# Kernel tuning notes

Measured on AMD Instinct MI355X. Metric: run time of the kernel, lower is better.

The kernel has to match this reference:

```python
import jax, jax.numpy as jnp
import numpy as np

B, CIN, COUT, L, K = 4, 512, 512, 4096, 7
DIL, STR = 1, 1
OUT_LEN = (L - DIL * (K - 1) - 1) // STR + 1  # 4090 ('valid' conv output length)


def setup_inputs() -> dict:
    key = jax.random.key(0)
    k1, k2, k3, k4 = jax.random.split(key, 4)
    x = jax.random.normal(k1, (B, CIN, L), dtype=jnp.float32)
    offsets = jax.random.normal(k2, (B, 1, OUT_LEN, K), dtype=jnp.float32)
    # kaiming_uniform_(a=sqrt(5)) on [COUT, CIN, K] -> U(-1/sqrt(fan_in), 1/sqrt(fan_in))
    fan_in = CIN * K
    bound = 1.0 / np.sqrt(fan_in)
    weight = jax.random.uniform(k3, (COUT, CIN, K), dtype=jnp.float32, minval=-bound, maxval=bound)
    bias = jax.random.uniform(k4, (COUT,), dtype=jnp.float32, minval=-bound, maxval=bound)
    return {"x": x, "offsets": offsets, "weight": weight, "bias": bias}


def _deform_interp(x, offsets, kernel_size, dilation, stride):
    # x: [B, C, L]; offsets: [B, 1, out_len, K] (offset_groups == 1)
    Lx = x.shape[-1]
    dil_pos = (jnp.arange(kernel_size) * dilation).astype(offsets.dtype)       # [K]
    out_len = offsets.shape[-2]
    t0s = (jnp.arange(out_len) * stride).astype(offsets.dtype)[:, None]        # [out_len, 1]
    T = t0s + dil_pos + offsets                                                # [B, 1, out_len, K]
    # constrained: each sample must stay inside its receptive field
    T = jnp.maximum(T, t0s)
    T = jnp.minimum(T, t0s + dil_pos[-1])
    U0 = jnp.clip(jnp.floor(T).astype(jnp.int32), 0, Lx - 2)                   # [B, 1, out_len, K]
    U = jnp.stack([U0, U0 + 1], axis=-1)                                       # [B, 1, out_len, K, 2]
    idx = U[:, 0]                                                              # [B, out_len, K, 2]
    # gather along length, broadcast index over channels
    xg = jax.vmap(lambda xb, ib: xb[:, ib])(x, idx)                            # [B, C, out_len, K, 2]
    # linear-interp weights: max(0, 1 - |U - T|)
    G = jnp.maximum(0.0, 1.0 - jnp.abs(U.astype(T.dtype) - T[..., None]))      # [B, 1, out_len, K, 2]
    return jnp.sum(G * xg, axis=-1)                                            # [B, C, out_len, K]


def reference(x, offsets, weight, bias):
    samp = _deform_interp(x, offsets, K, DIL, STR)                             # [B, C, out_len, K]
    # conv1d(weight, stride=K) on flattened [B, C, out_len*K] == per-position full contraction
    out = jnp.einsum('bcok,dck->bdo', samp, weight) + bias[:, None]            # [B, COUT, out_len]
    return out
```

## Files before the change

### kernel.cpp

```cpp
#include <hip/hip_runtime.h>
#include <hip/hip_bf16.h>
#include <stdint.h>

#define B_      4
#define CIN     512
#define COUT    512
#define L_      4096
#define K_      7
#define OUT_LEN 4090

typedef unsigned short ushort_t;
typedef __attribute__((ext_vector_type(8))) __bf16 bf16x8;
typedef __attribute__((ext_vector_type(4))) float f32x4;

__device__ __forceinline__ uint32_t f2bf(float f) {
    uint32_t u = __float_as_uint(f);
    return (u + 0x7fffu + ((u >> 16) & 1u)) >> 16;
}

__device__ __forceinline__ uint32_t pack2bf(float s0, float s1) {
    __hip_bfloat162 h = __float22bfloat162_rn(make_float2(s0, s1));
    uint32_t r;
    __builtin_memcpy(&r, &h, 4);
    return r;
}

__device__ __forceinline__ uint32_t interp1(uint32_t wl, uint32_t wh, float g0, float g1) {
    const float l0 = __uint_as_float(wl << 16);
    const float l1 = __uint_as_float(wl & 0xffff0000u);
    const float h0 = __uint_as_float(wh << 16);
    const float h1 = __uint_as_float(wh & 0xffff0000u);
    return pack2bf(g0 * l0 + g1 * h0, g0 * l1 + g1 * h1);
}

__device__ __forceinline__ void async16(const void* g, void* l) {
    __builtin_amdgcn_global_load_lds(
        (const __attribute__((address_space(1))) unsigned int*)g,
        (__attribute__((address_space(3))) unsigned int*)l, 16, 0, 0);
}


__global__ __launch_bounds__(256)
void reorder_w2_kernel(const float* __restrict__ w, uint32_t* __restrict__ Wr) {
    const int d   = blockIdx.x;
    const int tid = threadIdx.x;
    __shared__ float wrow[3584];
    const float4* src = (const float4*)(w + (size_t)d * 3584);
    for (int e = tid; e < 896; e += 256) ((float4*)wrow)[e] = src[e];
    __syncthreads();
    const int cc  = tid >> 4;
    const int clp = tid & 15;
    const int pos = (((clp >> 2) ^ ((d >> 1) & 3)) << 2) | (clp & 3);
    #pragma unroll
    for (int k = 0; k < K_; ++k) {
        const float w0 = wrow[tid * 14 + k];
        const float w1 = wrow[tid * 14 + 7 + k];
        Wr[((size_t)(cc * 7 + k) * 512 + d) * 16 + pos] = (f2bf(w1) << 16) | f2bf(w0);
    }
}

__global__ __launch_bounds__(256)
void interp_pack_kernel(const float* __restrict__ x, const float* __restrict__ offs,
                        uint32_t* __restrict__ P) {
    const int obx = blockIdx.x;
    const int cc  = blockIdx.y;
    const int b   = blockIdx.z;
    const int tid = threadIdx.x;
    const int o0  = obx * 128;
    __shared__ __align__(16) uint32_t XT[2176];

    const float* xc = x + ((size_t)b * CIN + cc * 32) * L_ + o0;
    #pragma unroll
    for (int r = 0; r < 3; ++r) {
        const int e = r * 256 + tid;
        if (e < 544) {
            const int cp   = e / 34;
            const int col4 = e - cp * 34;
            const int colb = col4 * 4;
            const float* p0 = xc + (size_t)(2 * cp) * L_ + colb;
            const float* p1 = p0 + L_;
            float4 v0, v1;
            if (o0 + colb + 3 < L_) {
                v0 = *(const float4*)p0;
                v1 = *(const float4*)p1;
            } else {
                float a0 = (o0 + colb + 0 < L_) ? p0[0] : 0.f;
                float a1 = (o0 + colb + 1 < L_) ? p0[1] : 0.f;
                float a2 = (o0 + colb + 2 < L_) ? p0[2] : 0.f;
                float a3 = (o0 + colb + 3 < L_) ? p0[3] : 0.f;
                float b0 = (o0 + colb + 0 < L_) ? p1[0] : 0.f;
                float b1 = (o0 + colb + 1 < L_) ? p1[1] : 0.f;
                float b2 = (o0 + colb + 2 < L_) ? p1[2] : 0.f;
                float b3 = (o0 + colb + 3 < L_) ? p1[3] : 0.f;
                v0 = make_float4(a0, a1, a2, a3);
                v1 = make_float4(b0, b1, b2, b3);
            }
            const float* f0 = (const float*)&v0;
            const float* f1 = (const float*)&v1;
            const int cpg = cp >> 1, hh = cp & 1;
            #pragma unroll
            for (int ii = 0; ii < 4; ++ii) {
                const int col = colb + ii;
                XT[col * 16 + (((cpg ^ (col & 7)) << 1) | hh)] = pack2bf(f0[ii], f1[ii]);
            }
        }
    }
    __syncthreads();

    const int o_loc = tid >> 1;
    const int h     = tid & 1;
    int o = o0 + o_loc; if (o > OUT_LEN - 1) o = OUT_LEN - 1;
    const float t0f = (float)o;
    const int sr = (o_loc >> 1) & 3;
    uint32_t* Pb = P + ((size_t)((b * 16 + cc) * 7) * 32 + obx) * 2048 + o_loc * 16;
    const int c0 = ((2 * h) ^ sr) << 2;
    const int c1 = ((2 * h + 1) ^ sr) << 2;
    #pragma unroll
    for (int k = 0; k < K_; ++k) {
        const float off = offs[((size_t)b * OUT_LEN + o) * K_ + k];
        float T = t0f + (float)k + off;
        T = fmaxf(T, t0f);
        T = fminf(T, t0f + 6.0f);
        int u0 = (int)floorf(T); if (u0 > L_ - 2) u0 = L_ - 2;
        const float g1 = T - (float)u0;
        const float g0 = 1.0f - g1;
        const int ul = u0 - o0;
        const uint32_t* R0 = &XT[ul * 16];
        const uint32_t* R1 = &XT[(ul + 1) * 16];
        const int s0 = ul & 7, s1 = (ul + 1) & 7;
        uint32_t ow[8];
        #pragma unroll
        for (int q = 0; q < 4; ++q) {
            const int pg = h * 4 + q;
            const uint2 lo = *(const uint2*)&R0[(pg ^ s0) << 1];
            const uint2 hi = *(const uint2*)&R1[(pg ^ s1) << 1];
            ow[q * 2 + 0] = interp1(lo.x, hi.x, g0, g1);
            ow[q * 2 + 1] = interp1(lo.y, hi.y, g0, g1);
        }
        uint32_t* Pk = Pb + (size_t)k * 65536;
        *(uint4*)&Pk[c0] = make_uint4(ow[0], ow[1], ow[2], ow[3]);
        *(uint4*)&Pk[c1] = make_uint4(ow[4], ow[5], ow[6], ow[7]);
    }
}

__global__ __launch_bounds__(256, 2)
void gemm_kernel(const ushort_t* __restrict__ Wr, const uint32_t* __restrict__ P,
                 const float* __restrict__ bias, float* __restrict__ out) {
    const int bxi  = blockIdx.x;
    const int o0   = bxi * 128;
    const int d0   = blockIdx.y * 128;
    const int b    = blockIdx.z;
    const int tid  = threadIdx.x;
    const int wv   = tid >> 6;
    const int lane = tid & 63;
    const int m16  = lane & 15;
    const int quad = lane >> 4;
    const int wd   = wv >> 1;
    const int wo   = wv & 1;
    const int sw   = (m16 >> 1) & 3;
    const int chk  = (quad ^ sw) * 8;

    __shared__ __align__(16) ushort_t As0[4096], As1[4096], As2[4096], As3[4096];
    __shared__ __align__(16) ushort_t Bs0[4096], Bs1[4096], Bs2[4096], Bs3[4096];

    const int aoff = (wd * 64 + m16) * 32 + chk;
    const int boff = (wo * 64 + m16) * 32 + chk;

    const ushort_t* Ag = Wr + (size_t)d0 * 32 + (size_t)tid * 8;
    const uint32_t* Bg = P + ((size_t)(b * 112) * 32 + bxi) * 2048 + (size_t)tid * 4;

#define NISSUE_A(S, ASP)                                                          \
    { _Pragma("unroll") for (int r_ = 0; r_ < 2; ++r_)                            \
        async16(Ag + (size_t)(S) * 16384 + r_ * 2048,                             \
                (void*)((ASP) + (r_ * 256 + wv * 64) * 8)); }

#define NISSUE_B(S, BSP)                                                          \
    { _Pragma("unroll") for (int r_ = 0; r_ < 2; ++r_)                            \
        async16(Bg + (size_t)(S) * 65536 + r_ * 1024,                             \
                (void*)((BSP) + (r_ * 256 + wv * 64) * 8)); }

#define NSTEP(ASP, BSP)                                                           \
    {                                                                             \
        bf16x8 af_[4], bf_[4];                                                    \
        _Pragma("unroll")                                                         \
        for (int i_ = 0; i_ < 4; ++i_) af_[i_] = *(const bf16x8*)&(ASP)[aoff + i_ * 512]; \
        _Pragma("unroll")                                                         \
        for (int j_ = 0; j_ < 4; ++j_) bf_[j_] = *(const bf16x8*)&(BSP)[boff + j_ * 512]; \
        _Pragma("unroll")                                                         \
        for (int i_ = 0; i_ < 4; ++i_) {                                          \
            _Pragma("unroll")                                                     \
            for (int j_ = 0; j_ < 4; ++j_)                                        \
                acc[i_][j_] = __builtin_amdgcn_mfma_f32_16x16x32_bf16(af_[i_], bf_[j_], acc[i_][j_], 0, 0, 0); \
        }                                                                         \
    }

    f32x4 acc[4][4];
    #pragma unroll
    for (int i = 0; i < 4; ++i) {
        #pragma unroll
        for (int j = 0; j < 4; ++j) acc[i][j] = (f32x4){0.f, 0.f, 0.f, 0.f};
    }

    NISSUE_A(0, As0); NISSUE_B(0, Bs0);
    NISSUE_A(1, As1); NISSUE_B(1, Bs1);
    __syncthreads();

    #pragma unroll 1
    for (int s = 0; s < 112; s += 8) {
        NISSUE_A(s + 2, As2); NISSUE_B(s + 2, Bs2); NISSUE_A(s + 3, As3); NISSUE_B(s + 3, Bs3);
        NSTEP(As0, Bs0); NSTEP(As1, Bs1); __syncthreads();
        NISSUE_A(s + 4, As0); NISSUE_B(s + 4, Bs0); NISSUE_A(s + 5, As1); NISSUE_B(s + 5, Bs1);
        NSTEP(As2, Bs2); NSTEP(As3, Bs3); __syncthreads();
        NISSUE_A(s + 6, As2); NISSUE_B(s + 6, Bs2); NISSUE_A(s + 7, As3); NISSUE_B(s + 7, Bs3);
        NSTEP(As0, Bs0); NSTEP(As1, Bs1); __syncthreads();
        if (s + 8 < 112) {
            NISSUE_A(s + 8, As0); NISSUE_B(s + 8, Bs0); NISSUE_A(s + 9, As1); NISSUE_B(s + 9, Bs1);
        }
        NSTEP(As2, Bs2); NSTEP(As3, Bs3); __syncthreads();
    }

    #pragma unroll
    for (int i = 0; i < 4; ++i) {
        const int dd = d0 + wd * 64 + i * 16 + quad * 4;
        float bv[4];
        #pragma unroll
        for (int r = 0; r < 4; ++r) bv[r] = bias[dd + r];
        #pragma unroll
        for (int j = 0; j < 4; ++j) {
            const int oo = o0 + wo * 64 + j * 16 + m16;
            if (oo < OUT_LEN) {
                float* op = out + (size_t)b * COUT * OUT_LEN + (size_t)dd * OUT_LEN + oo;
                #pragma unroll
                for (int r = 0; r < 4; ++r)
                    op[(size_t)r * OUT_LEN] = acc[i][j][r] + bv[r];
            }
        }
    }
#undef NISSUE_A
#undef NISSUE_B
#undef NSTEP
}


__global__ __launch_bounds__(256)
void reorder_w1_kernel(const float* __restrict__ w, uint32_t* __restrict__ Wr) {
    const int d   = blockIdx.x;
    const int tid = threadIdx.x;
    __shared__ float wrow[3584];
    const float4* src = (const float4*)(w + (size_t)d * 3584);
    for (int e = tid; e < 896; e += 256) ((float4*)wrow)[e] = src[e];
    __syncthreads();
    const int cc  = tid >> 4;
    const int clp = tid & 15;
    #pragma unroll
    for (int k = 0; k < K_; ++k) {
        const float w0 = wrow[tid * 14 + k];
        const float w1 = wrow[tid * 14 + 7 + k];
        Wr[((size_t)((k * 16 + cc) * 512 + d)) * 16 + clp] = (f2bf(w1) << 16) | f2bf(w0);
    }
}

__global__ __launch_bounds__(256)
void prepack_kernel(const float* __restrict__ x, uint32_t* __restrict__ xpack) {
    const int obx = blockIdx.x;
    const int cc  = blockIdx.y;
    const int b   = blockIdx.z;
    const int tid = threadIdx.x;
    const int o0  = obx * 128;
    __shared__ __align__(16) uint32_t XT[2176];
    const float* xc = x + ((size_t)b * CIN + cc * 32) * L_ + o0;
    #pragma unroll
    for (int r = 0; r < 3; ++r) {
        const int e = r * 256 + tid;
        if (e < 544) {
            const int cp   = e / 34;
            const int col4 = e - cp * 34;
            const int colb = col4 * 4;
            const float* p0 = xc + (size_t)(2 * cp) * L_ + colb;
            const float* p1 = p0 + L_;
            float4 v0, v1;
            if (o0 + colb + 3 < L_) {
                v0 = *(const float4*)p0;
                v1 = *(const float4*)p1;
            } else {
                float a0 = (o0 + colb + 0 < L_) ? p0[0] : 0.f;
                float a1 = (o0 + colb + 1 < L_) ? p0[1] : 0.f;
                float a2 = (o0 + colb + 2 < L_) ? p0[2] : 0.f;
                float a3 = (o0 + colb + 3 < L_) ? p0[3] : 0.f;
                float b0 = (o0 + colb + 0 < L_) ? p1[0] : 0.f;
                float b1 = (o0 + colb + 1 < L_) ? p1[1] : 0.f;
                float b2 = (o0 + colb + 2 < L_) ? p1[2] : 0.f;
                float b3 = (o0 + colb + 3 < L_) ? p1[3] : 0.f;
                v0 = make_float4(a0, a1, a2, a3);
                v1 = make_float4(b0, b1, b2, b3);
            }
            const float* f0 = (const float*)&v0;
            const float* f1 = (const float*)&v1;
            const int cpg = cp >> 1, h = cp & 1;
            #pragma unroll
            for (int ii = 0; ii < 4; ++ii) {
                const int col = colb + ii;
                XT[col * 16 + (((cpg ^ (col & 7)) << 1) | h)] = pack2bf(f0[ii], f1[ii]);
            }
        }
    }
    __syncthreads();
    uint4* dst = (uint4*)xpack + (size_t)((b * 16 + cc) * 32 + obx) * 544;
    const uint4* s4 = (const uint4*)XT;
    #pragma unroll
    for (int r = 0; r < 3; ++r) {
        const int e = r * 256 + tid;
        if (e < 544) dst[e] = s4[e];
    }
}

__global__ __launch_bounds__(256, 2)
void fused_v1_kernel(const float* __restrict__ offs, const ushort_t* __restrict__ Wr,
                     const uint32_t* __restrict__ xpack, const float* __restrict__ bias,
                     float* __restrict__ out) {
    const int bxi  = blockIdx.x;
    const int o0   = bxi * 128;
    const int d0   = blockIdx.y * 128;
    const int b    = blockIdx.z;
    const int tid  = threadIdx.x;
    const int wv   = tid >> 6;
    const int lane = tid & 63;
    const int m16  = lane & 15;
    const int quad = lane >> 4;
    const int ob   = wv * 32;
    const int q2   = quad * 2;

    __shared__ __align__(16) ushort_t As0[4096], As1[4096], As2[4096], As3[4096];
    __shared__ __align__(16) uint32_t XTB0[2304], XTB1[2304];
    __shared__ int    SU[896];
    __shared__ float2 PG[896];

#define ISSUE_A(KK, CC, ASP)                                                      \
    {                                                                             \
        _Pragma("unroll")                                                         \
        for (int r_ = 0; r_ < 2; ++r_) {                                          \
            const int c_ = r_ * 256 + tid;                                        \
            const int row_ = c_ >> 2, pc_ = c_ & 3;                               \
            const ushort_t* g_ = Wr                                               \
                + ((size_t)(((KK) * 16 + (CC)) * 512 + d0 + row_)) * 32 + pc_ * 8;\
            async16(g_, (void*)((ASP) + (r_ * 256 + wv * 64) * 8));               \
        }                                                                         \
    }

#define ISSUE_XTB(CC, XP)                                                         \
    {                                                                             \
        const uint32_t* sp_ = xpack + ((size_t)((b * 16 + (CC)) * 32 + bxi)) * 2176; \
        _Pragma("unroll")                                                         \
        for (int r_ = 0; r_ < 3; ++r_) {                                          \
            const int cb_ = r_ * 256 + wv * 64;                                   \
            if (cb_ < 544) {                                                      \
                const int c_ = r_ * 256 + tid;                                    \
                async16((const void*)(sp_ + (size_t)c_ * 4),                      \
                        (void*)((XP) + (size_t)cb_ * 4));                         \
            }                                                                     \
        }                                                                         \
    }

#define STEP(KK, XP, ASP)                                                         \
    {                                                                             \
        bf16x8 af_[8];                                                            \
        _Pragma("unroll")                                                         \
        for (int i_ = 0; i_ < 8; ++i_)                                            \
            af_[i_] = *(const bf16x8*)&(ASP)[(i_ * 16 + m16) * 32 + quad * 8];    \
        bf16x8 bfr_[2];                                                           \
        _Pragma("unroll")                                                         \
        for (int j_ = 0; j_ < 2; ++j_) {                                          \
            const int row_ = ((KK) << 7) | (ob + j_ * 16 + m16);                  \
            const int u_ = SU[row_];                                              \
            const float2 g_ = PG[row_];                                           \
            const uint32_t* Xr0_ = &(XP)[u_ * 16];                                \
            const uint32_t* Xr1_ = Xr0_ + 16;                                     \
            const int s0_ = u_ & 7, s1_ = (u_ + 1) & 7;                           \
            const uint2 a0_ = *(const uint2*)&Xr0_[((q2     ^ s0_) << 1)];        \
            const uint2 a1_ = *(const uint2*)&Xr0_[(((q2+1) ^ s0_) << 1)];        \
            const uint2 c0_ = *(const uint2*)&Xr1_[((q2     ^ s1_) << 1)];        \
            const uint2 c1_ = *(const uint2*)&Xr1_[(((q2+1) ^ s1_) << 1)];        \
            uint4 rr_;                                                            \
            rr_.x = interp1(a0_.x, c0_.x, g_.x, g_.y);                            \
            rr_.y = interp1(a0_.y, c0_.y, g_.x, g_.y);                            \
            rr_.z = interp1(a1_.x, c1_.x, g_.x, g_.y);                            \
            rr_.w = interp1(a1_.y, c1_.y, g_.x, g_.y);                            \
            __builtin_memcpy(&bfr_[j_], &rr_, 16);                                \
        }                                                                         \
        _Pragma("unroll")                                                         \
        for (int i_ = 0; i_ < 8; ++i_) {                                          \
            _Pragma("unroll")                                                     \
            for (int j_ = 0; j_ < 2; ++j_)                                        \
                acc[i_][j_] = __builtin_amdgcn_mfma_f32_16x16x32_bf16(af_[i_], bfr_[j_], acc[i_][j_], 0, 0, 0); \
        }                                                                         \
    }

#define HALF(CCB, A0_, A1_, A2_, A3_)                                             \
    ISSUE_A(2, (CCB), A2_); ISSUE_A(3, (CCB), A3_); ISSUE_XTB((CCB) + 1, XTB1);   \
    STEP(0, XTB0, A0_); STEP(1, XTB0, A1_); __syncthreads();                      \
    ISSUE_A(4, (CCB), A0_); ISSUE_A(5, (CCB), A1_);                               \
    STEP(2, XTB0, A2_); STEP(3, XTB0, A3_); __syncthreads();                      \
    ISSUE_A(6, (CCB), A2_); ISSUE_A(0, (CCB) + 1, A3_);                           \
    STEP(4, XTB0, A0_); STEP(5, XTB0, A1_); __syncthreads();                      \
    ISSUE_A(1, (CCB) + 1, A0_); ISSUE_A(2, (CCB) + 1, A1_);                       \
    STEP(6, XTB0, A2_); STEP(0, XTB1, A3_); __syncthreads();                      \
    ISSUE_A(3, (CCB) + 1, A2_); ISSUE_A(4, (CCB) + 1, A3_);                       \
    if ((CCB) + 2 < 16) { ISSUE_XTB((CCB) + 2, XTB0); }                           \
    STEP(1, XTB1, A0_); STEP(2, XTB1, A1_); __syncthreads();                      \
    ISSUE_A(5, (CCB) + 1, A0_); ISSUE_A(6, (CCB) + 1, A1_);                       \
    STEP(3, XTB1, A2_); STEP(4, XTB1, A3_); __syncthreads();                      \
    if ((CCB) + 2 < 16) { ISSUE_A(0, (CCB) + 2, A2_); ISSUE_A(1, (CCB) + 2, A3_); } \
    STEP(5, XTB1, A0_); STEP(6, XTB1, A1_); __syncthreads();

    f32x4 acc[8][2];
    #pragma unroll
    for (int i = 0; i < 8; ++i) {
        #pragma unroll
        for (int j = 0; j < 2; ++j) acc[i][j] = (f32x4){0.f, 0.f, 0.f, 0.f};
    }

    ISSUE_XTB(0, XTB0);
    ISSUE_A(0, 0, As0);
    ISSUE_A(1, 0, As1);
    for (int e = tid; e < 896; e += 256) {
        const int k  = e >> 7;
        const int ol = e & 127;
        int o = o0 + ol; if (o > OUT_LEN - 1) o = OUT_LEN - 1;
        const float t0  = (float)o;
        const float off = offs[((size_t)b * OUT_LEN + o) * K_ + k];
        float T = t0 + (float)k + off;
        T = fmaxf(T, t0);
        T = fminf(T, t0 + 6.0f);
        int u0 = (int)floorf(T);
        if (u0 > L_ - 2) u0 = L_ - 2;
        const float g0 = fmaxf(1.0f - fabsf((float)u0 - T), 0.0f);
        const float g1 = fmaxf(1.0f - fabsf((float)(u0 + 1) - T), 0.0f);
        SU[e] = u0 - o0;
        PG[e] = make_float2(g0, g1);
    }
    __syncthreads();

    #pragma unroll 1
    for (int s4 = 0; s4 < 16; s4 += 4) {
        HALF(s4,     As0, As1, As2, As3)
        HALF(s4 + 2, As2, As3, As0, As1)
    }

    #pragma unroll
    for (int i = 0; i < 8; ++i) {
        const int dd = d0 + i * 16 + quad * 4;
        float bv[4];
        #pragma unroll
        for (int r = 0; r < 4; ++r) bv[r] = bias[dd + r];
        #pragma unroll
        for (int j = 0; j < 2; ++j) {
            const int oo = o0 + ob + j * 16 + m16;
            if (oo < OUT_LEN) {
                float* op = out + (size_t)b * COUT * OUT_LEN + (size_t)dd * OUT_LEN + oo;
                #pragma unroll
                for (int r = 0; r < 4; ++r)
                    op[(size_t)r * OUT_LEN] = acc[i][j][r] + bv[r];
            }
        }
    }
#undef ISSUE_A
#undef ISSUE_XTB
#undef STEP
#undef HALF
}

#define BM 64
#define BN 64
#define BC 8
#define TT (BC * K_)

__global__ __launch_bounds__(256, 2)
void deform_conv1d_fallback(const float* __restrict__ x, const float* __restrict__ offsets,
                            const float* __restrict__ weight, const float* __restrict__ bias,
                            float* __restrict__ out) {
    const int o0 = blockIdx.x * BN, d0 = blockIdx.y * BM, b = blockIdx.z, tid = threadIdx.x;
    __shared__ int   SU[BN * K_];
    __shared__ float SG0[BN * K_], SG1[BN * K_];
    __shared__ float XT[BC][BN + 8];
    __shared__ float S[BC][K_][BN];
    __shared__ float WT[BM][TT + 1];
    for (int e = tid; e < BN * K_; e += 256) {
        const int ol = e / K_, k = e % K_, o = o0 + ol;
        int u0rel = 0; float g0 = 0.f, g1 = 0.f;
        if (o < OUT_LEN) {
            const float t0 = (float)o;
            const float off = offsets[(size_t)b * OUT_LEN * K_ + (size_t)o * K_ + k];
            float T = fminf(fmaxf(t0 + (float)k + off, t0), t0 + 6.0f);
            int u0 = (int)floorf(T); if (u0 > L_ - 2) u0 = L_ - 2;
            g0 = fmaxf(1.0f - fabsf((float)u0 - T), 0.0f);
            g1 = fmaxf(1.0f - fabsf((float)(u0 + 1) - T), 0.0f);
            u0rel = u0 - o0;
        }
        SU[e] = u0rel; SG0[e] = g0; SG1[e] = g1;
    }
    float acc[4][4];
    #pragma unroll
    for (int i = 0; i < 4; ++i) {
        #pragma unroll
        for (int j = 0; j < 4; ++j) acc[i][j] = 0.f;
    }
    const int ty = tid >> 4, tx = tid & 15;
    const float* xb = x + (size_t)b * CIN * L_;
    for (int c0 = 0; c0 < CIN; c0 += BC) {
        __syncthreads();
        for (int e = tid; e < BC * (BN + 7); e += 256) {
            const int cl = e / (BN + 7), j = e % (BN + 7), pos = o0 + j;
            XT[cl][j] = (pos < L_) ? xb[(size_t)(c0 + cl) * L_ + pos] : 0.f;
        }
        for (int e = tid; e < BM * TT; e += 256) {
            const int d = e / TT, t = e % TT;
            WT[d][t] = weight[(size_t)(d0 + d) * (CIN * K_) + c0 * K_ + t];
        }
        __syncthreads();
        for (int e = tid; e < BC * K_ * BN; e += 256) {
            const int cl = e / (K_ * BN), r = e % (K_ * BN), k = r / BN, ol = r % BN;
            const int p = ol * K_ + k, u = SU[p];
            S[cl][k][ol] = SG0[p] * XT[cl][u] + SG1[p] * XT[cl][u + 1];
        }
        __syncthreads();
        #pragma unroll
        for (int t = 0; t < TT; ++t) {
            const int cl = t / K_, k = t % K_;
            const float4 s4 = *(const float4*)&S[cl][k][tx * 4];
            const float w0 = WT[ty * 4 + 0][t], w1 = WT[ty * 4 + 1][t];
            const float w2 = WT[ty * 4 + 2][t], w3 = WT[ty * 4 + 3][t];
            acc[0][0] += w0 * s4.x; acc[0][1] += w0 * s4.y; acc[0][2] += w0 * s4.z; acc[0][3] += w0 * s4.w;
            acc[1][0] += w1 * s4.x; acc[1][1] += w1 * s4.y; acc[1][2] += w1 * s4.z; acc[1][3] += w1 * s4.w;
            acc[2][0] += w2 * s4.x; acc[2][1] += w2 * s4.y; acc[2][2] += w2 * s4.z; acc[2][3] += w2 * s4.w;
            acc[3][0] += w3 * s4.x; acc[3][1] += w3 * s4.y; acc[3][2] += w3 * s4.z; acc[3][3] += w3 * s4.w;
        }
    }
    #pragma unroll
    for (int i = 0; i < 4; ++i) {
        const int d = d0 + ty * 4 + i;
        const float bvv = bias[d];
        #pragma unroll
        for (int j = 0; j < 4; ++j) {
            const int o = o0 + tx * 4 + j;
            if (o < OUT_LEN)
                out[(size_t)b * COUT * OUT_LEN + (size_t)d * OUT_LEN + o] = acc[i][j] + bvv;
        }
    }
}

extern "C" void kernel_launch(void* const* d_in, const int* in_sizes, int n_in,
                              void* d_out, int out_size, void* d_ws, size_t ws_size,
                              hipStream_t stream) {
    const float* x       = (const float*)d_in[0];
    const float* offsets = (const float*)d_in[1];
    const float* weight  = (const float*)d_in[2];
    const float* bias    = (const float*)d_in[3];
    float* out = (float*)d_out;

    const size_t WR_BYTES = (size_t)512 * 512 * 7 * 2;
    const size_t P_BYTES  = (size_t)4 * 16 * 7 * 32 * 8192;
    const size_t XP_BYTES = (size_t)2048 * 544 * 16 + 512;

    if (ws_size >= WR_BYTES + P_BYTES) {
        uint32_t* Wr_u32 = (uint32_t*)d_ws;
        ushort_t* Wr     = (ushort_t*)d_ws;
        uint32_t* P      = (uint32_t*)((char*)d_ws + WR_BYTES);
        reorder_w2_kernel<<<512, 256, 0, stream>>>(weight, Wr_u32);
        interp_pack_kernel<<<dim3(32, 16, B_), 256, 0, stream>>>(x, offsets, P);
        gemm_kernel<<<dim3(32, 4, B_), 256, 0, stream>>>(Wr, P, bias, out);
        return;
    }

    if (ws_size >= WR_BYTES + XP_BYTES) {
        uint32_t* Wr_u32 = (uint32_t*)d_ws;
        ushort_t* Wr     = (ushort_t*)d_ws;
        uint32_t* xpack  = (uint32_t*)((char*)d_ws + WR_BYTES);
        reorder_w1_kernel<<<512, 256, 0, stream>>>(weight, Wr_u32);
        prepack_kernel<<<dim3(32, 16, B_), 256, 0, stream>>>(x, xpack);
        fused_v1_kernel<<<dim3(32, 4, B_), 256, 0, stream>>>(offsets, Wr, xpack, bias, out);
        return;
    }

    dim3 grid((OUT_LEN + BN - 1) / BN, COUT / BM, B_);
    deform_conv1d_fallback<<<grid, 256, 0, stream>>>(x, offsets, weight, bias, out);
}
```

Measured before the change: 171.1 us.

## Load GEMM fragments directly from global memory into registers, dropping LDS staging

The GEMM kernel no longer stages A and B tiles through four LDS buffers with async copies and block barriers. Each wave now loads its bf16 MFMA fragments straight from global memory into registers, double-buffered one k-step ahead, and raises wave priority around the MFMA bursts. This removes LDS traffic and __syncthreads, but each tile is now fetched by several waves without sharing, which adds global/L2 traffic and exposes more load latency.

```diff
diff --git a/kernel.cpp b/kernel.cpp
--- a/kernel.cpp
+++ b/kernel.cpp
@@ -158,41 +158,30 @@
     const int wd   = wv >> 1;
     const int wo   = wv & 1;
     const int sw   = (m16 >> 1) & 3;
-    const int chk  = (quad ^ sw) * 8;
-
-    __shared__ __align__(16) ushort_t As0[4096], As1[4096], As2[4096], As3[4096];
-    __shared__ __align__(16) ushort_t Bs0[4096], Bs1[4096], Bs2[4096], Bs3[4096];
-
-    const int aoff = (wd * 64 + m16) * 32 + chk;
-    const int boff = (wo * 64 + m16) * 32 + chk;
-
-    const ushort_t* Ag = Wr + (size_t)d0 * 32 + (size_t)tid * 8;
-    const uint32_t* Bg = P + ((size_t)(b * 112) * 32 + bxi) * 2048 + (size_t)tid * 4;
-
-#define NISSUE_A(S, ASP)                                                          \
-    { _Pragma("unroll") for (int r_ = 0; r_ < 2; ++r_)                            \
-        async16(Ag + (size_t)(S) * 16384 + r_ * 2048,                             \
-                (void*)((ASP) + (r_ * 256 + wv * 64) * 8)); }
-
-#define NISSUE_B(S, BSP)                                                          \
-    { _Pragma("unroll") for (int r_ = 0; r_ < 2; ++r_)                            \
-        async16(Bg + (size_t)(S) * 65536 + r_ * 1024,                             \
-                (void*)((BSP) + (r_ * 256 + wv * 64) * 8)); }
-
-#define NSTEP(ASP, BSP)                                                           \
-    {                                                                             \
-        bf16x8 af_[4], bf_[4];                                                    \
-        _Pragma("unroll")                                                         \
-        for (int i_ = 0; i_ < 4; ++i_) af_[i_] = *(const bf16x8*)&(ASP)[aoff + i_ * 512]; \
-        _Pragma("unroll")                                                         \
-        for (int j_ = 0; j_ < 4; ++j_) bf_[j_] = *(const bf16x8*)&(BSP)[boff + j_ * 512]; \
-        _Pragma("unroll")                                                         \
-        for (int i_ = 0; i_ < 4; ++i_) {                                          \
-            _Pragma("unroll")                                                     \
-            for (int j_ = 0; j_ < 4; ++j_)                                        \
-                acc[i_][j_] = __builtin_amdgcn_mfma_f32_16x16x32_bf16(af_[i_], bf_[j_], acc[i_][j_], 0, 0, 0); \
-        }                                                                         \
-    }
+    const int chk  = quad ^ sw;
+
+    const ushort_t* Ab = Wr + (size_t)(d0 + wd * 64 + m16) * 32 + chk * 8;
+    const uint32_t* Bb = P + ((size_t)(b * 112) * 32 + bxi) * 2048
+                           + (wo * 64 + m16) * 16 + chk * 4;
+
+#define LDF(AF, BF, S)                                                        \
+    { _Pragma("unroll")                                                       \
+      for (int i_ = 0; i_ < 4; ++i_)                                          \
+          AF[i_] = *(const bf16x8*)(Ab + (size_t)(S) * 16384 + i_ * 512);     \
+      _Pragma("unroll")                                                       \
+      for (int j_ = 0; j_ < 4; ++j_)                                          \
+          BF[j_] = *(const bf16x8*)(Bb + (size_t)(S) * 65536 + j_ * 256); }
+
+#define MFMA16(AF, BF)                                                        \
+    { __builtin_amdgcn_s_setprio(1);                                          \
+      _Pragma("unroll")                                                       \
+      for (int i_ = 0; i_ < 4; ++i_) {                                        \
+          _Pragma("unroll")                                                   \
+          for (int j_ = 0; j_ < 4; ++j_)                                      \
+              acc[i_][j_] = __builtin_amdgcn_mfma_f32_16x16x32_bf16(          \
+                  AF[i_], BF[j_], acc[i_][j_], 0, 0, 0);                      \
+      }                                                                       \
+      __builtin_amdgcn_s_setprio(0); }
 
     f32x4 acc[4][4];
     #pragma unroll
@@ -201,23 +190,18 @@
         for (int j = 0; j < 4; ++j) acc[i][j] = (f32x4){0.f, 0.f, 0.f, 0.f};
     }
 
-    NISSUE_A(0, As0); NISSUE_B(0, Bs0);
-    NISSUE_A(1, As1); NISSUE_B(1, Bs1);
-    __syncthreads();
-
+    bf16x8 aC[4], bC[4], aN[4], bN[4];
+    LDF(aC, bC, 0);
     #pragma unroll 1
-    for (int s = 0; s < 112; s += 8) {
-        NISSUE_A(s + 2, As2); NISSUE_B(s + 2, Bs2); NISSUE_A(s + 3, As3); NISSUE_B(s + 3, Bs3);
-        NSTEP(As0, Bs0); NSTEP(As1, Bs1); __syncthreads();
-        NISSUE_A(s + 4, As0); NISSUE_B(s + 4, Bs0); NISSUE_A(s + 5, As1); NISSUE_B(s + 5, Bs1);
-        NSTEP(As2, Bs2); NSTEP(As3, Bs3); __syncthreads();
-        NISSUE_A(s + 6, As2); NISSUE_B(s + 6, Bs2); NISSUE_A(s + 7, As3); NISSUE_B(s + 7, Bs3);
-        NSTEP(As0, Bs0); NSTEP(As1, Bs1); __syncthreads();
-        if (s + 8 < 112) {
-            NISSUE_A(s + 8, As0); NISSUE_B(s + 8, Bs0); NISSUE_A(s + 9, As1); NISSUE_B(s + 9, Bs1);
-        }
-        NSTEP(As2, Bs2); NSTEP(As3, Bs3); __syncthreads();
-    }
+    for (int s = 0; s < 110; s += 2) {
+        LDF(aN, bN, s + 1);
+        MFMA16(aC, bC);
+        LDF(aC, bC, s + 2);
+        MFMA16(aN, bN);
+    }
+    LDF(aN, bN, 111);
+    MFMA16(aC, bC);
+    MFMA16(aN, bN);
 
     #pragma unroll
     for (int i = 0; i < 4; ++i) {
@@ -236,9 +220,8 @@
             }
         }
     }
-#undef NISSUE_A
-#undef NISSUE_B
-#undef NSTEP
+#undef LDF
+#undef MFMA16
 }
 
 
```

Result: slower. 182.4 us (+6.6%).

## Use per-stage vmcnt waits and barriers with MFMA priority in GEMM main loop

Applied to the files above, without the earlier changes.

The GEMM main loop used to sync once every two stages with __syncthreads, which waits for all outstanding async loads. It now barriers once per stage and waits only with s_waitcnt vmcnt(8), so the two most recent stages' loads stay in flight while the current buffer is consumed. The loop ends with an explicit epilogue that drains the queue. The MFMA block is also wrapped in s_setprio to favour compute issue. This gives deeper load/compute overlap in exchange for more barriers and hand-counted wait values that must match the number of loads issued per stage.

```diff
diff --git a/kernel.cpp b/kernel.cpp
--- a/kernel.cpp
+++ b/kernel.cpp
@@ -169,29 +169,35 @@
     const ushort_t* Ag = Wr + (size_t)d0 * 32 + (size_t)tid * 8;
     const uint32_t* Bg = P + ((size_t)(b * 112) * 32 + bxi) * 2048 + (size_t)tid * 4;
 
-#define NISSUE_A(S, ASP)                                                          \
-    { _Pragma("unroll") for (int r_ = 0; r_ < 2; ++r_)                            \
-        async16(Ag + (size_t)(S) * 16384 + r_ * 2048,                             \
-                (void*)((ASP) + (r_ * 256 + wv * 64) * 8)); }
-
-#define NISSUE_B(S, BSP)                                                          \
-    { _Pragma("unroll") for (int r_ = 0; r_ < 2; ++r_)                            \
-        async16(Bg + (size_t)(S) * 65536 + r_ * 1024,                             \
+#define ISSUE(S, ASP, BSP)                                                    \
+    { _Pragma("unroll") for (int r_ = 0; r_ < 2; ++r_)                        \
+        async16(Ag + (size_t)(S) * 16384 + r_ * 2048,                         \
+                (void*)((ASP) + (r_ * 256 + wv * 64) * 8));                   \
+      _Pragma("unroll") for (int r_ = 0; r_ < 2; ++r_)                        \
+        async16(Bg + (size_t)(S) * 65536 + r_ * 1024,                         \
                 (void*)((BSP) + (r_ * 256 + wv * 64) * 8)); }
 
-#define NSTEP(ASP, BSP)                                                           \
-    {                                                                             \
-        bf16x8 af_[4], bf_[4];                                                    \
-        _Pragma("unroll")                                                         \
+#define WAITBAR(N)                                                            \
+    { asm volatile("s_waitcnt vmcnt(" #N ")" ::: "memory");                   \
+      __builtin_amdgcn_s_barrier();                                           \
+      __builtin_amdgcn_sched_barrier(0); }
+
+#define SSTEP(ASP, BSP)                                                       \
+    {                                                                         \
+        bf16x8 af_[4], bf_[4];                                                \
+        _Pragma("unroll")                                                     \
         for (int i_ = 0; i_ < 4; ++i_) af_[i_] = *(const bf16x8*)&(ASP)[aoff + i_ * 512]; \
-        _Pragma("unroll")                                                         \
+        _Pragma("unroll")                                                     \
         for (int j_ = 0; j_ < 4; ++j_) bf_[j_] = *(const bf16x8*)&(BSP)[boff + j_ * 512]; \
-        _Pragma("unroll")                                                         \
-        for (int i_ = 0; i_ < 4; ++i_) {                                          \
-            _Pragma("unroll")                                                     \
-            for (int j_ = 0; j_ < 4; ++j_)                                        \
-                acc[i_][j_] = __builtin_amdgcn_mfma_f32_16x16x32_bf16(af_[i_], bf_[j_], acc[i_][j_], 0, 0, 0); \
-        }                                                                         \
+        __builtin_amdgcn_s_setprio(1);                                        \
+        _Pragma("unroll")                                                     \
+        for (int i_ = 0; i_ < 4; ++i_) {                                      \
+            _Pragma("unroll")                                                 \
+            for (int j_ = 0; j_ < 4; ++j_)                                    \
+                acc[i_][j_] = __builtin_amdgcn_mfma_f32_16x16x32_bf16(        \
+                    af_[i_], bf_[j_], acc[i_][j_], 0, 0, 0);                  \
+        }                                                                     \
+        __builtin_amdgcn_s_setprio(0);                                        \
     }
 
     f32x4 acc[4][4];
@@ -201,23 +207,20 @@
         for (int j = 0; j < 4; ++j) acc[i][j] = (f32x4){0.f, 0.f, 0.f, 0.f};
     }
 
-    NISSUE_A(0, As0); NISSUE_B(0, Bs0);
-    NISSUE_A(1, As1); NISSUE_B(1, Bs1);
-    __syncthreads();
+    ISSUE(0, As0, Bs0);
+    ISSUE(1, As1, Bs1);
 
     #pragma unroll 1
-    for (int s = 0; s < 112; s += 8) {
-        NISSUE_A(s + 2, As2); NISSUE_B(s + 2, Bs2); NISSUE_A(s + 3, As3); NISSUE_B(s + 3, Bs3);
-        NSTEP(As0, Bs0); NSTEP(As1, Bs1); __syncthreads();
-        NISSUE_A(s + 4, As0); NISSUE_B(s + 4, Bs0); NISSUE_A(s + 5, As1); NISSUE_B(s + 5, Bs1);
-        NSTEP(As2, Bs2); NSTEP(As3, Bs3); __syncthreads();
-        NISSUE_A(s + 6, As2); NISSUE_B(s + 6, Bs2); NISSUE_A(s + 7, As3); NISSUE_B(s + 7, Bs3);
-        NSTEP(As0, Bs0); NSTEP(As1, Bs1); __syncthreads();
-        if (s + 8 < 112) {
-            NISSUE_A(s + 8, As0); NISSUE_B(s + 8, Bs0); NISSUE_A(s + 9, As1); NISSUE_B(s + 9, Bs1);
-        }
-        NSTEP(As2, Bs2); NSTEP(As3, Bs3); __syncthreads();
-    }
+    for (int t = 0; t < 108; t += 4) {
+        ISSUE(t + 2, As2, Bs2); WAITBAR(8); SSTEP(As0, Bs0);
+        ISSUE(t + 3, As3, Bs3); WAITBAR(8); SSTEP(As1, Bs1);
+        ISSUE(t + 4, As0, Bs0); WAITBAR(8); SSTEP(As2, Bs2);
+        ISSUE(t + 5, As1, Bs1); WAITBAR(8); SSTEP(As3, Bs3);
+    }
+    ISSUE(110, As2, Bs2); WAITBAR(8); SSTEP(As0, Bs0);
+    ISSUE(111, As3, Bs3); WAITBAR(8); SSTEP(As1, Bs1);
+    WAITBAR(4); SSTEP(As2, Bs2);
+    WAITBAR(0); SSTEP(As3, Bs3);
 
     #pragma unroll
     for (int i = 0; i < 4; ++i) {
@@ -236,9 +239,9 @@
             }
         }
     }
-#undef NISSUE_A
-#undef NISSUE_B
-#undef NSTEP
+#undef ISSUE
+#undef WAITBAR
+#undef SSTEP
 }
 
 
```

Result: no change. 169.1 us (-1.2%).
